# Kernel tuning notes

Measured on AMD Instinct MI355X. Metric: run time of the kernel, lower is better.

The kernel has to match this reference:

```python
import jax, jax.numpy as jnp
import numpy as np

N = 200000
H = 128        # n_heads == input feature dim
HID = 512      # hidden_features
D_H = 512      # scaling denominator
C = 10.0       # tanh clip scale


def setup_inputs() -> dict:
    key = jax.random.key(0)
    k0, k1, k2, k3, k4, k5 = jax.random.split(key, 6)
    output = jax.random.normal(k0, (N, H), dtype=jnp.float32)
    # adjacency row: binary mask (which nodes are reachable neighbors)
    adj_modified = (jax.random.uniform(k1, (N,)) < 0.5).astype(jnp.float32)
    W1 = jax.random.normal(k2, (HID, H), dtype=jnp.float32) * (1.0 / np.sqrt(H))
    b1 = jax.random.normal(k3, (HID,), dtype=jnp.float32) * 0.01
    W2 = jax.random.normal(k4, (HID, H), dtype=jnp.float32) * (1.0 / np.sqrt(H))
    b2 = jax.random.normal(k5, (HID,), dtype=jnp.float32) * 0.01
    return {"output": output, "adj_modified": adj_modified,
            "W1": W1, "b1": b1, "W2": W2, "b2": b2, "prev_node": 5}


def reference(output, adj_modified, W1, b1, W2, b2, prev_node):
    # v_i: [1, H] embedding of the previously selected node
    v_i = output[prev_node][None, :]
    # v_j: [N, H] neighbor embeddings gated by the adjacency row
    v_j = adj_modified[:, None] * output
    phi1_v_i = v_i @ W1.T + b1          # [1, HID]
    phi2_v_j = v_j @ W2.T + b2          # [N, HID]
    scores = (phi1_v_i @ phi2_v_j.T) / jnp.sqrt(jnp.asarray(D_H, jnp.float32))  # [1, N]
    attn = C * jnp.tanh(scores) * adj_modified  # clipped + masked, [1, N]
    attn = attn[0]                                # [N]
    w = jax.nn.softmax(attn, axis=0)
    w = w * (attn != 0).astype(w.dtype)
    p = w.max()
    selected_node = jnp.argmax(w)
    return selected_node, p
```

## Files before the change

### kernel.cpp

```cpp
#include <hip/hip_runtime.h>
#include <math.h>

#define H 128
#define HID 512
#define GRID 2048

struct Ws {
    float s_b;
    float pad;
    float u[H];
    unsigned long long best_part[GRID];
    float Z_part[GRID];
};

__device__ __forceinline__ unsigned int fkey(float f) {
    unsigned int u = __float_as_uint(f);
    return (u & 0x80000000u) ? ~u : (u | 0x80000000u);
}
__device__ __forceinline__ float inv_fkey(unsigned int k) {
    return __uint_as_float((k & 0x80000000u) ? (k ^ 0x80000000u) : ~k);
}

__global__ __launch_bounds__(1024)
void prep_kernel(const float* __restrict__ outp, const float* __restrict__ W1,
                 const float* __restrict__ b1, const float* __restrict__ W2,
                 const float* __restrict__ b2, const int* __restrict__ prev,
                 Ws* __restrict__ ws) {
    __shared__ float phi1_s[HID];
    __shared__ float sb_s[32];
    __shared__ float u_part[8][H];
    int t = threadIdx.x;
    int lane = t & 63;
    int c = lane & 31;
    int g = t >> 5;
    const float4* vi = (const float4*)(outp + (size_t)prev[0] * H);
    float4 v = vi[c];
    float sb = 0.f;
#pragma unroll 4
    for (int r = 0; r < 16; ++r) {
        int k = g * 16 + r;
        float4 w = ((const float4*)(W1 + (size_t)k * H))[c];
        float d = w.x * v.x + w.y * v.y + w.z * v.z + w.w * v.w;
        d += __shfl_xor(d, 16);
        d += __shfl_xor(d, 8);
        d += __shfl_xor(d, 4);
        d += __shfl_xor(d, 2);
        d += __shfl_xor(d, 1);
        if (c == 0) {
            float phi = d + b1[k];
            phi1_s[k] = phi;
            sb += phi * b2[k];
        }
    }
    if (c == 0) sb_s[g] = sb;
    __syncthreads();
    int h = t & 127;
    int g2 = t >> 7;
    float up = 0.f;
#pragma unroll 8
    for (int kk = 0; kk < 64; ++kk) {
        int k = g2 * 64 + kk;
        up += phi1_s[k] * W2[(size_t)k * H + h];
    }
    u_part[g2][h] = up;
    __syncthreads();
    if (t < H) {
        float s = 0.f;
#pragma unroll
        for (int i = 0; i < 8; ++i) s += u_part[i][h];
        ws->u[h] = s;
    }
    if (t == 0) {
        float s = 0.f;
#pragma unroll
        for (int i = 0; i < 32; ++i) s += sb_s[i];
        ws->s_b = s;
    }
}

__global__ __launch_bounds__(256)
void score_kernel(const float4* __restrict__ xv, const float* __restrict__ adj,
                  Ws* __restrict__ ws, int n, int ntiles) {
    __shared__ float zs[4];
    __shared__ unsigned long long bs[4];
    const float inv = 0.04419417382415922f;
    int t = threadIdx.x;
    int lane = t & 63;
    int c = lane & 31;
    int hv = lane >> 5;
    int w = t >> 6;
    float s_b = ws->s_b;
    float4 uv = ((const float4*)ws->u)[c];
    float zloc = 0.f;
    float bscore = -3.4e38f;
    int bidx = -1;
    for (int tile = blockIdx.x; tile < ntiles; tile += GRID) {
        int base = tile * 32 + w * 8 + hv;
        float4 x[4];
#pragma unroll
        for (int r = 0; r < 4; ++r) {
            int row = base + 2 * r;
            if (row >= n) row = n - 1;
            x[r] = xv[(size_t)row * 32 + c];
        }
        float d[4];
#pragma unroll
        for (int r = 0; r < 4; ++r) {
            float dd = x[r].x * uv.x + x[r].y * uv.y + x[r].z * uv.z + x[r].w * uv.w;
            dd += __shfl_xor(dd, 16);
            dd += __shfl_xor(dd, 8);
            dd += __shfl_xor(dd, 4);
            dd += __shfl_xor(dd, 2);
            dd += __shfl_xor(dd, 1);
            d[r] = dd;
        }
        if (c < 4) {
            int row = base + 2 * c;
            if (row < n) {
                float dm = d[0];
#pragma unroll
                for (int r = 1; r < 4; ++r) dm = (c == r) ? d[r] : dm;
                float a = adj[row];
                float attn = 0.f;
                if (a != 0.f) {
                    float score = (s_b + a * dm) * inv;
                    float e = __expf(2.f * score);
                    attn = 10.f * ((e - 1.f) / (e + 1.f));
                    if (score > bscore) { bscore = score; bidx = row; }
                }
                zloc += __expf(attn);
            }
        }
    }
#pragma unroll
    for (int m = 32; m >= 1; m >>= 1) zloc += __shfl_xor(zloc, m);
    unsigned long long pk = 0ull;
    if (bidx >= 0)
        pk = ((unsigned long long)fkey(bscore) << 32) |
             (unsigned long long)(0xFFFFFFFFu - (unsigned int)bidx);
#pragma unroll
    for (int m = 32; m >= 1; m >>= 1) {
        unsigned long long o = __shfl_xor(pk, m);
        if (o > pk) pk = o;
    }
    if (lane == 0) { zs[w] = zloc; bs[w] = pk; }
    __syncthreads();
    if (t == 0) {
        float z = zs[0] + zs[1] + zs[2] + zs[3];
        unsigned long long p2 = bs[0];
#pragma unroll
        for (int i = 1; i < 4; ++i) if (bs[i] > p2) p2 = bs[i];
        ws->Z_part[blockIdx.x] = z;
        ws->best_part[blockIdx.x] = p2;
    }
}

__global__ __launch_bounds__(1024)
void reduce_kernel(const Ws* __restrict__ ws, float* __restrict__ outp) {
    __shared__ float zs[16];
    __shared__ unsigned long long bs[16];
    int t = threadIdx.x;
    int lane = t & 63;
    float z = ws->Z_part[t] + ws->Z_part[t + 1024];
    unsigned long long pk = ws->best_part[t];
    unsigned long long o2 = ws->best_part[t + 1024];
    if (o2 > pk) pk = o2;
#pragma unroll
    for (int m = 32; m >= 1; m >>= 1) {
        z += __shfl_xor(z, m);
        unsigned long long o = __shfl_xor(pk, m);
        if (o > pk) pk = o;
    }
    if (lane == 0) { zs[t >> 6] = z; bs[t >> 6] = pk; }
    __syncthreads();
    if (t == 0) {
        float Z = 0.f;
        unsigned long long b = 0ull;
#pragma unroll
        for (int i = 0; i < 16; ++i) { Z += zs[i]; if (bs[i] > b) b = bs[i]; }
        unsigned int idx = 0xFFFFFFFFu - (unsigned int)(b & 0xFFFFFFFFu);
        float score = inv_fkey((unsigned int)(b >> 32));
        float p = __expf(10.f * tanhf(score)) / Z;
        if (b == 0ull) { idx = 0; p = 0.f; }
        outp[0] = (float)idx;
        outp[1] = p;
    }
}

extern "C" void kernel_launch(void* const* d_in, const int* in_sizes, int n_in,
                              void* d_out, int out_size, void* d_ws, size_t ws_size,
                              hipStream_t stream) {
    const float* outp = (const float*)d_in[0];
    const float* adj  = (const float*)d_in[1];
    const float* W1   = (const float*)d_in[2];
    const float* b1   = (const float*)d_in[3];
    const float* W2   = (const float*)d_in[4];
    const float* b2   = (const float*)d_in[5];
    const int*   prev = (const int*)d_in[6];
    int n = in_sizes[1];
    Ws* ws = (Ws*)d_ws;

    int ntiles = (n + 31) / 32;

    prep_kernel<<<1, 1024, 0, stream>>>(outp, W1, b1, W2, b2, prev, ws);
    score_kernel<<<GRID, 256, 0, stream>>>((const float4*)outp, adj, ws, n, ntiles);
    reduce_kernel<<<1, 1024, 0, stream>>>(ws, (float*)d_out);
}
```

Before: 185.1 us.

## Split prep kernel across 16 blocks and reduce partial vectors in score kernel

The single-block prep kernel, which computes u = W2^T·phi1 and the bias term s_b, is split across 16 blocks of 256 threads, each covering 32 hidden units. Each block writes partial u and s_b sums to the workspace, and every score block adds up the 16 partials on load. The goal is to shorten the serial prep stage, which runs on one CU, at the cost of a few extra loads and adds per score block.

```diff
diff --git a/kernel.cpp b/kernel.cpp
--- a/kernel.cpp
+++ b/kernel.cpp
@@ -4,11 +4,11 @@
 #define H 128
 #define HID 512
 #define GRID 2048
+#define PREP_B 16
 
 struct Ws {
-    float s_b;
-    float pad;
-    float u[H];
+    float sb_part[PREP_B];
+    float u_part[PREP_B][H];
     unsigned long long best_part[GRID];
     float Z_part[GRID];
 };
@@ -21,24 +21,26 @@
     return __uint_as_float((k & 0x80000000u) ? (k ^ 0x80000000u) : ~k);
 }
 
-__global__ __launch_bounds__(1024)
+__global__ __launch_bounds__(256)
 void prep_kernel(const float* __restrict__ outp, const float* __restrict__ W1,
                  const float* __restrict__ b1, const float* __restrict__ W2,
                  const float* __restrict__ b2, const int* __restrict__ prev,
                  Ws* __restrict__ ws) {
-    __shared__ float phi1_s[HID];
-    __shared__ float sb_s[32];
-    __shared__ float u_part[8][H];
+    __shared__ float phi1_s[32];
+    __shared__ float sb_s[8];
+    __shared__ float u_s[2][H];
     int t = threadIdx.x;
     int lane = t & 63;
     int c = lane & 31;
     int g = t >> 5;
+    int kbase = blockIdx.x * 32;
     const float4* vi = (const float4*)(outp + (size_t)prev[0] * H);
     float4 v = vi[c];
     float sb = 0.f;
-#pragma unroll 4
-    for (int r = 0; r < 16; ++r) {
-        int k = g * 16 + r;
+#pragma unroll
+    for (int r = 0; r < 4; ++r) {
+        int kl = g * 4 + r;
+        int k = kbase + kl;
         float4 w = ((const float4*)(W1 + (size_t)k * H))[c];
         float d = w.x * v.x + w.y * v.y + w.z * v.z + w.w * v.w;
         d += __shfl_xor(d, 16);
@@ -48,7 +50,7 @@
         d += __shfl_xor(d, 1);
         if (c == 0) {
             float phi = d + b1[k];
-            phi1_s[k] = phi;
+            phi1_s[kl] = phi;
             sb += phi * b2[k];
         }
     }
@@ -57,24 +59,19 @@
     int h = t & 127;
     int g2 = t >> 7;
     float up = 0.f;
-#pragma unroll 8
-    for (int kk = 0; kk < 64; ++kk) {
-        int k = g2 * 64 + kk;
-        up += phi1_s[k] * W2[(size_t)k * H + h];
-    }
-    u_part[g2][h] = up;
-    __syncthreads();
-    if (t < H) {
-        float s = 0.f;
-#pragma unroll
-        for (int i = 0; i < 8; ++i) s += u_part[i][h];
-        ws->u[h] = s;
-    }
+#pragma unroll
+    for (int kk = 0; kk < 16; ++kk) {
+        int kl = g2 * 16 + kk;
+        up += phi1_s[kl] * W2[(size_t)(kbase + kl) * H + h];
+    }
+    u_s[g2][h] = up;
+    __syncthreads();
+    if (t < H) ws->u_part[blockIdx.x][t] = u_s[0][t] + u_s[1][t];
     if (t == 0) {
         float s = 0.f;
 #pragma unroll
-        for (int i = 0; i < 32; ++i) s += sb_s[i];
-        ws->s_b = s;
+        for (int i = 0; i < 8; ++i) s += sb_s[i];
+        ws->sb_part[blockIdx.x] = s;
     }
 }
 
@@ -89,8 +86,14 @@
     int c = lane & 31;
     int hv = lane >> 5;
     int w = t >> 6;
-    float s_b = ws->s_b;
-    float4 uv = ((const float4*)ws->u)[c];
+    float4 uv = make_float4(0.f, 0.f, 0.f, 0.f);
+    float s_b = 0.f;
+#pragma unroll
+    for (int b = 0; b < PREP_B; ++b) {
+        float4 p = ((const float4*)ws->u_part[b])[c];
+        uv.x += p.x; uv.y += p.y; uv.z += p.z; uv.w += p.w;
+        s_b += ws->sb_part[b];
+    }
     float zloc = 0.f;
     float bscore = -3.4e38f;
     int bidx = -1;
@@ -202,7 +205,7 @@
 
     int ntiles = (n + 31) / 32;
 
-    prep_kernel<<<1, 1024, 0, stream>>>(outp, W1, b1, W2, b2, prev, ws);
+    prep_kernel<<<PREP_B, 256, 0, stream>>>(outp, W1, b1, W2, b2, prev, ws);
     score_kernel<<<GRID, 256, 0, stream>>>((const float4*)outp, adj, ws, n, ntiles);
     reduce_kernel<<<1, 1024, 0, stream>>>(ws, (float*)d_out);
 }
```

Result: faster. 169.0 us (-8.7%).
